# Kernel tuning notes

Measured on AMD Instinct MI355X. Metric: run time of the kernel, lower is better.

## Reference

```python
import jax, jax.numpy as jnp
import numpy as np

N = 50000    # num nodes
E = 800000   # num edges
B = 256      # num graphs
AD, BD = 39, 10          # atom / bond feature dims
H, HEADS, HD, L, TD = 128, 4, 32, 3, 128  # hidden, heads, head_dim, layers, time_dim
BN_EPS = 1e-5


def setup_inputs() -> dict:
    key = jax.random.key(0)
    ks = jax.random.split(key, 24)
    g = lambda i, shape: jax.random.normal(ks[i], shape, dtype=jnp.float32) * 0.05
    return {
        "x": jax.random.normal(ks[0], (N, AD), dtype=jnp.float32),
        "edge_index": jax.random.randint(ks[1], (2, E), 0, N),
        "edge_attr": jax.random.normal(ks[2], (E, BD), dtype=jnp.float32),
        "batch": jnp.sort(jax.random.randint(ks[3], (N,), 0, B)),
        "t": jax.random.randint(ks[4], (B,), 0, 1000),
        "atom_W": g(5, (AD, H)), "atom_b": jnp.zeros((H,), jnp.float32),
        "bond_W": g(6, (BD, H)), "bond_b": jnp.zeros((H,), jnp.float32),
        "lin_W": g(7, (L, H, H)), "edge_W": g(8, (L, H, H)),
        "att_src": g(9, (L, HEADS, HD)), "att_dst": g(10, (L, HEADS, HD)),
        "att_edge": g(11, (L, HEADS, HD)), "conv_b": jnp.zeros((L, H), jnp.float32),
        "bn_gamma": jnp.ones((L, H), jnp.float32), "bn_beta": jnp.zeros((L, H), jnp.float32),
        "out_W": g(12, (H, H)), "out_b": jnp.zeros((H,), jnp.float32),
        "time_W1": g(13, (TD, H)), "time_b1": jnp.zeros((H,), jnp.float32),
        "time_W2": g(14, (H, H)), "time_b2": jnp.zeros((H,), jnp.float32),
        "pool_W1": g(15, (H, H)), "pool_b1": jnp.zeros((H,), jnp.float32),
        "pool_W2": g(16, (H, H)), "pool_b2": jnp.zeros((H,), jnp.float32),
        "np_W1": g(17, (2 * H, H)), "np_b1": jnp.zeros((H,), jnp.float32),
        "np_W2": g(18, (H, H)), "np_b2": jnp.zeros((H,), jnp.float32),
        "np_W3": g(19, (H, AD)), "np_b3": jnp.zeros((AD,), jnp.float32),
    }


def _time_embedding(tf):
    half = TD // 2
    freqs = jnp.exp(jnp.arange(half, dtype=jnp.float32) * (-np.log(10000.0) / (half - 1)))
    e = tf[:, None] * freqs[None, :]
    return jnp.concatenate([jnp.sin(e), jnp.cos(e)], axis=-1)


def _gat_layer(h, e_emb, src, dst, W, We, a_src, a_dst, a_edge, bias):
    # PyG GATConv: shared lin for src/dst, edge features modulate attention only.
    xh = (h @ W).reshape(N, HEADS, HD)
    eh = (e_emb @ We).reshape(E, HEADS, HD)
    s_src = jnp.sum(xh * a_src, axis=-1)    # [N, HEADS]
    s_dst = jnp.sum(xh * a_dst, axis=-1)    # [N, HEADS]
    s_edge = jnp.sum(eh * a_edge, axis=-1)  # [E, HEADS]
    alpha = jax.nn.leaky_relu(s_src[src] + s_dst[dst] + s_edge, 0.2)  # [E, HEADS]
    amax = jax.ops.segment_max(alpha, dst, num_segments=N)
    amax = jnp.where(jnp.isfinite(amax), amax, 0.0)
    ea = jnp.exp(alpha - amax[dst])
    denom = jax.ops.segment_sum(ea, dst, num_segments=N)
    w = ea / (denom[dst] + 1e-16)           # segment softmax over incoming edges
    msg = xh[src] * w[:, :, None]           # [E, HEADS, HD]
    return jax.ops.segment_sum(msg, dst, num_segments=N).reshape(N, H) + bias


def reference(x, edge_index, edge_attr, batch, t,
              atom_W, atom_b, bond_W, bond_b,
              lin_W, edge_W, att_src, att_dst, att_edge, conv_b, bn_gamma, bn_beta,
              out_W, out_b, time_W1, time_b1, time_W2, time_b2,
              pool_W1, pool_b1, pool_W2, pool_b2,
              np_W1, np_b1, np_W2, np_b2, np_W3, np_b3):
    src, dst = edge_index[0], edge_index[1]
    # time conditioning
    t_emb = _time_embedding(t.astype(jnp.float32))
    t_emb = jax.nn.silu(t_emb @ time_W1 + time_b1) @ time_W2 + time_b2  # [B, H]
    # GNN backbone
    h = x @ atom_W + atom_b
    e_emb = edge_attr @ bond_W + bond_b
    for i in range(L):
        h_in = h
        h = _gat_layer(h, e_emb, src, dst, lin_W[i], edge_W[i],
                       att_src[i], att_dst[i], att_edge[i], conv_b[i])
        mu = h.mean(axis=0)
        var = h.var(axis=0)
        h = (h - mu) / jnp.sqrt(var + BN_EPS) * bn_gamma[i] + bn_beta[i]
        h = jax.nn.relu(h)
        h = h + h_in  # residual (dropout is eval-mode identity)
    node_features = h @ out_W + out_b  # [N, H]
    # graph mean pool + pooling MLP
    counts = jnp.clip(jax.ops.segment_sum(jnp.ones((N,), h.dtype), batch, num_segments=B), 1.0, None)
    graph = jax.ops.segment_sum(node_features, batch, num_segments=B) / counts[:, None]
    graph = jax.nn.silu(graph @ pool_W1 + pool_b1) @ pool_W2 + pool_b2  # [B, H]
    tg = t_emb + graph
    # per-node noise prediction
    z = jnp.concatenate([node_features, tg[batch]], axis=-1)  # [N, 2H]
    z = jax.nn.silu(z @ np_W1 + np_b1)
    z = jax.nn.silu(z @ np_W2 + np_b2)
    return z @ np_W3 + np_b3  # [N, AD]
```

## Files before the change

kernel.cpp:

```cpp
#include <hip/hip_runtime.h>
#include <hip/hip_fp16.h>
#include <math.h>

#define N_NODES 50000
#define N_EDGES 800000
#define NB 256
#define AD 39
#define BD 10
#define H 128
#define HEADS 4
#define HD 32
#define LAYERS 3
#define TD 128
#define NBUCK 196
#define EPB 4096

typedef _Float16 f16x8 __attribute__((ext_vector_type(8)));
typedef float f32x4 __attribute__((ext_vector_type(4)));

__device__ __forceinline__ float silu_f(float x) { return x / (1.f + __expf(-x)); }

__device__ __forceinline__ void fma_rank1(float acc[8][4], float4 aL, float4 aH, float4 w)
{
    float ar[8] = {aL.x, aL.y, aL.z, aL.w, aH.x, aH.y, aH.z, aH.w};
    float wr[4] = {w.x, w.y, w.z, w.w};
#pragma unroll
    for (int r = 0; r < 8; r++)
#pragma unroll
        for (int j = 0; j < 4; j++) acc[r][j] += ar[r] * wr[j];
}

template<int KT>
__global__ __launch_bounds__(256) void gemm128(
    const float* __restrict__ A, const float* __restrict__ W,
    const float* __restrict__ bias, float* __restrict__ out,
    int Nrows, int ldw)
{
    __shared__ float As[KT * 68];
    const int tid = threadIdx.x;
    const int rowBase = blockIdx.x * 64;

    for (int idx = tid; idx < 64 * KT; idx += 256) {
        int row = idx / KT;
        int k = idx - row * KT;
        int n = rowBase + row;
        As[k * 68 + row] = (n < Nrows) ? A[(size_t)n * KT + k] : 0.f;
    }
    __syncthreads();

    const int c0 = (tid & 31) * 4;
    const int n0 = (tid >> 5) * 8;

    float acc[8][4];
#pragma unroll
    for (int r = 0; r < 8; r++)
#pragma unroll
        for (int j = 0; j < 4; j++) acc[r][j] = 0.f;

    const float* wp = W + c0;
    int k = 0;
    for (; k + 4 <= KT; k += 4) {
        float4 w0 = *(const float4*)&wp[(size_t)(k + 0) * ldw];
        float4 w1 = *(const float4*)&wp[(size_t)(k + 1) * ldw];
        float4 w2 = *(const float4*)&wp[(size_t)(k + 2) * ldw];
        float4 w3 = *(const float4*)&wp[(size_t)(k + 3) * ldw];
        float4 aL0 = *(const float4*)&As[(k + 0) * 68 + n0];
        float4 aH0 = *(const float4*)&As[(k + 0) * 68 + n0 + 4];
        float4 aL1 = *(const float4*)&As[(k + 1) * 68 + n0];
        float4 aH1 = *(const float4*)&As[(k + 1) * 68 + n0 + 4];
        float4 aL2 = *(const float4*)&As[(k + 2) * 68 + n0];
        float4 aH2 = *(const float4*)&As[(k + 2) * 68 + n0 + 4];
        float4 aL3 = *(const float4*)&As[(k + 3) * 68 + n0];
        float4 aH3 = *(const float4*)&As[(k + 3) * 68 + n0 + 4];
        fma_rank1(acc, aL0, aH0, w0);
        fma_rank1(acc, aL1, aH1, w1);
        fma_rank1(acc, aL2, aH2, w2);
        fma_rank1(acc, aL3, aH3, w3);
    }
    for (; k < KT; ++k) {
        float4 w0 = *(const float4*)&wp[(size_t)k * ldw];
        float4 aL = *(const float4*)&As[k * 68 + n0];
        float4 aH = *(const float4*)&As[k * 68 + n0 + 4];
        fma_rank1(acc, aL, aH, w0);
    }

    float4 bv = make_float4(0.f, 0.f, 0.f, 0.f);
    if (bias) bv = *(const float4*)&bias[c0];

#pragma unroll
    for (int r = 0; r < 8; r++) {
        int n = rowBase + n0 + r;
        if (n >= Nrows) break;
        float4 o;
        o.x = acc[r][0] + bv.x;
        o.y = acc[r][1] + bv.y;
        o.z = acc[r][2] + bv.z;
        o.w = acc[r][3] + bv.w;
        *(float4*)&out[(size_t)n * H + c0] = o;
    }
}

__global__ __launch_bounds__(256) void convert_w_frags(
    const float* __restrict__ lin_W, const float* __restrict__ out_W,
    __half* __restrict__ w16)
{
    int tid = blockIdx.x * 256 + threadIdx.x;
    if (tid >= 4 * H * H) return;
    int mat = tid >> 14;
    int rem = tid & 16383;
    int k = rem >> 7;
    int n = rem & 127;
    const float* src = (mat < 3) ? (lin_W + (size_t)mat * H * H) : out_W;
    float v = src[(size_t)k * H + n];
    int ks = k >> 5, kr = k & 31;
    int lane = ((kr >> 3) << 4) | (n & 15);
    int j = kr & 7;
    int nb = n >> 4;
    w16[(size_t)mat * 16384 + (((ks * 8 + nb) * 64 + lane) << 3) + j] = __float2half(v);
}

__global__ __launch_bounds__(256) void convert_np_frags(
    const float* __restrict__ npW1, const float* __restrict__ npW2,
    const float* __restrict__ npW3, __half* __restrict__ wnp)
{
    int tid = blockIdx.x * 256 + threadIdx.x;
    const int TOT12 = 2 * H * H;
    if (tid < TOT12) {
        int mat = tid >> 14;
        int rem = tid & 16383;
        int k = rem >> 7;
        int n = rem & 127;
        const float* src = mat ? npW2 : npW1;
        float v = src[(size_t)k * H + n];
        int ks = k >> 5, kr = k & 31;
        int lane = ((kr >> 3) << 4) | (n & 15);
        int j = kr & 7;
        int nb = n >> 4;
        wnp[(size_t)mat * 16384 + (((ks * 8 + nb) * 64 + lane) << 3) + j] = __float2half(v);
    } else {
        int r = tid - TOT12;
        if (r >= H * 48) return;
        int k = r / 48;
        int n = r - k * 48;
        float v = (n < AD) ? npW3[(size_t)k * AD + n] : 0.f;
        int ks = k >> 5, kr = k & 31;
        int lane = ((kr >> 3) << 4) | (n & 15);
        int j = kr & 7;
        int nb = n >> 4;
        wnp[32768 + (((ks * 3 + nb) * 64 + lane) << 3) + j] = __float2half(v);
    }
}

__global__ __launch_bounds__(256) void gemm_mfma_bn(
    const float* __restrict__ A,
    const __half* __restrict__ agg, const float* __restrict__ scale,
    const float* __restrict__ shift, float* __restrict__ hio,
    const __half* __restrict__ wfrag, const float* __restrict__ bias,
    float* __restrict__ out32, __half* __restrict__ out16,
    const float* __restrict__ attS, const float* __restrict__ attD,
    float* __restrict__ sS, float* __restrict__ sD, int Nrows)
{
    __shared__ __half Ah[64 * 136];
    const int tid = threadIdx.x;
    const int rowBase = blockIdx.x * 64;

    for (int idx = tid; idx < 64 * 32; idx += 256) {
        int row = idx >> 5;
        int kq = (idx & 31) * 4;
        int n = rowBase + row;
        float4 v = make_float4(0.f, 0.f, 0.f, 0.f);
        if (n < Nrows) {
            if (agg) {
                uint2 u = *(const uint2*)&agg[(size_t)n * H + kq];
                float2 lo = __half22float2(*(__half2*)&u.x);
                float2 hi = __half22float2(*(__half2*)&u.y);
                float4 sc = *(const float4*)&scale[kq];
                float4 sh = *(const float4*)&shift[kq];
                float4 hv = *(const float4*)&hio[(size_t)n * H + kq];
                v.x = fmaxf(lo.x * sc.x + sh.x, 0.f) + hv.x;
                v.y = fmaxf(lo.y * sc.y + sh.y, 0.f) + hv.y;
                v.z = fmaxf(hi.x * sc.z + sh.z, 0.f) + hv.z;
                v.w = fmaxf(hi.y * sc.w + sh.w, 0.f) + hv.w;
                *(float4*)&hio[(size_t)n * H + kq] = v;
            } else {
                v = *(const float4*)&A[(size_t)n * H + kq];
            }
        }
        __half2 a = __floats2half2_rn(v.x, v.y);
        __half2 b = __floats2half2_rn(v.z, v.w);
        *(uint2*)&Ah[row * 136 + kq] = make_uint2(*(unsigned*)&a, *(unsigned*)&b);
    }
    __syncthreads();

    const int wave = tid >> 6;
    const int lane = tid & 63;
    const int lrow = lane & 15;
    const int lgrp = lane >> 4;

    f16x8 bf[4][2];
#pragma unroll
    for (int ks = 0; ks < 4; ks++)
#pragma unroll
        for (int nt = 0; nt < 2; nt++) {
            int nb = wave * 2 + nt;
            bf[ks][nt] = *(const f16x8*)&wfrag[(((ks * 8 + nb) * 64 + lane) << 3)];
        }

    f32x4 acc[4][2];
#pragma unroll
    for (int mt = 0; mt < 4; mt++)
#pragma unroll
        for (int nt = 0; nt < 2; nt++) acc[mt][nt] = (f32x4){0.f, 0.f, 0.f, 0.f};

#pragma unroll
    for (int ks = 0; ks < 4; ks++) {
#pragma unroll
        for (int mt = 0; mt < 4; mt++) {
            f16x8 af = *(const f16x8*)&Ah[(mt * 16 + lrow) * 136 + ks * 32 + lgrp * 8];
            acc[mt][0] = __builtin_amdgcn_mfma_f32_16x16x32_f16(af, bf[ks][0], acc[mt][0], 0, 0, 0);
            acc[mt][1] = __builtin_amdgcn_mfma_f32_16x16x32_f16(af, bf[ks][1], acc[mt][1], 0, 0, 0);
        }
    }

    const int col0 = wave * 32 + lrow;
    const int col1 = col0 + 16;
    float b0 = bias ? bias[col0] : 0.f;
    float b1 = bias ? bias[col1] : 0.f;
    float aS0 = 0.f, aS1 = 0.f, aD0 = 0.f, aD1 = 0.f;
    if (sS) {
        aS0 = attS[col0]; aS1 = attS[col1];
        aD0 = attD[col0]; aD1 = attD[col1];
    }

#pragma unroll
    for (int mt = 0; mt < 4; mt++) {
#pragma unroll
        for (int reg = 0; reg < 4; reg++) {
            int row = rowBase + mt * 16 + lgrp * 4 + reg;
            float v0 = acc[mt][0][reg] + b0;
            float v1 = acc[mt][1][reg] + b1;
            if (row < Nrows) {
                if (out16) {
                    out16[(size_t)row * H + col0] = __float2half(v0);
                    out16[(size_t)row * H + col1] = __float2half(v1);
                } else {
                    out32[(size_t)row * H + col0] = v0;
                    out32[(size_t)row * H + col1] = v1;
                }
            }
            if (sS) {
                float ps = v0 * aS0 + v1 * aS1;
                float pd = v0 * aD0 + v1 * aD1;
#pragma unroll
                for (int off = 8; off >= 1; off >>= 1) {
                    ps += __shfl_xor(ps, off, 16);
                    pd += __shfl_xor(pd, off, 16);
                }
                if (lrow == 0 && row < Nrows) {
                    sS[row * 4 + wave] = ps;
                    sD[row * 4 + wave] = pd;
                }
            }
        }
    }
}

__global__ __launch_bounds__(256) void np_fused_mfma(
    const float* __restrict__ nf, const int* __restrict__ batch,
    const float* __restrict__ tgW, const __half* __restrict__ wnp,
    const float* __restrict__ npb2, const float* __restrict__ npb3,
    float* __restrict__ out, int Nrows)
{
    __shared__ __half Ah[64 * 136];
    const int tid = threadIdx.x;
    const int rowBase = blockIdx.x * 64;

    for (int idx = tid; idx < 64 * 32; idx += 256) {
        int row = idx >> 5;
        int kq = (idx & 31) * 4;
        int n = rowBase + row;
        float4 v = make_float4(0.f, 0.f, 0.f, 0.f);
        if (n < Nrows) v = *(const float4*)&nf[(size_t)n * H + kq];
        __half2 a = __floats2half2_rn(v.x, v.y);
        __half2 b = __floats2half2_rn(v.z, v.w);
        *(uint2*)&Ah[row * 136 + kq] = make_uint2(*(unsigned*)&a, *(unsigned*)&b);
    }
    __syncthreads();

    const int wave = tid >> 6;
    const int lane = tid & 63;
    const int lrow = lane & 15;
    const int lgrp = lane >> 4;

    f32x4 acc[4][2];

    {
        f16x8 bf[4][2];
#pragma unroll
        for (int ks = 0; ks < 4; ks++)
#pragma unroll
            for (int nt = 0; nt < 2; nt++) {
                int nb = wave * 2 + nt;
                bf[ks][nt] = *(const f16x8*)&wnp[(((ks * 8 + nb) * 64 + lane) << 3)];
            }
#pragma unroll
        for (int mt = 0; mt < 4; mt++)
#pragma unroll
            for (int nt = 0; nt < 2; nt++) acc[mt][nt] = (f32x4){0.f, 0.f, 0.f, 0.f};
#pragma unroll
        for (int ks = 0; ks < 4; ks++) {
#pragma unroll
            for (int mt = 0; mt < 4; mt++) {
                f16x8 af = *(const f16x8*)&Ah[(mt * 16 + lrow) * 136 + ks * 32 + lgrp * 8];
                acc[mt][0] = __builtin_amdgcn_mfma_f32_16x16x32_f16(af, bf[ks][0], acc[mt][0], 0, 0, 0);
                acc[mt][1] = __builtin_amdgcn_mfma_f32_16x16x32_f16(af, bf[ks][1], acc[mt][1], 0, 0, 0);
            }
        }
    }
    __syncthreads();

#pragma unroll
    for (int mt = 0; mt < 4; mt++) {
#pragma unroll
        for (int nt = 0; nt < 2; nt++) {
            int col = wave * 32 + nt * 16 + lrow;
#pragma unroll
            for (int reg = 0; reg < 4; reg++) {
                int row = mt * 16 + lgrp * 4 + reg;
                int n = rowBase + row;
                float v = acc[mt][nt][reg];
                if (n < Nrows) v += tgW[(size_t)batch[n] * H + col];
                Ah[row * 136 + col] = __float2half(silu_f(v));
            }
        }
    }
    __syncthreads();

    {
        const __half* w2 = wnp + 16384;
        f16x8 bf[4][2];
#pragma unroll
        for (int ks = 0; ks < 4; ks++)
#pragma unroll
            for (int nt = 0; nt < 2; nt++) {
                int nb = wave * 2 + nt;
                bf[ks][nt] = *(const f16x8*)&w2[(((ks * 8 + nb) * 64 + lane) << 3)];
            }
#pragma unroll
        for (int mt = 0; mt < 4; mt++)
#pragma unroll
            for (int nt = 0; nt < 2; nt++) acc[mt][nt] = (f32x4){0.f, 0.f, 0.f, 0.f};
#pragma unroll
        for (int ks = 0; ks < 4; ks++) {
#pragma unroll
            for (int mt = 0; mt < 4; mt++) {
                f16x8 af = *(const f16x8*)&Ah[(mt * 16 + lrow) * 136 + ks * 32 + lgrp * 8];
                acc[mt][0] = __builtin_amdgcn_mfma_f32_16x16x32_f16(af, bf[ks][0], acc[mt][0], 0, 0, 0);
                acc[mt][1] = __builtin_amdgcn_mfma_f32_16x16x32_f16(af, bf[ks][1], acc[mt][1], 0, 0, 0);
            }
        }
    }
    __syncthreads();

#pragma unroll
    for (int mt = 0; mt < 4; mt++) {
#pragma unroll
        for (int nt = 0; nt < 2; nt++) {
            int col = wave * 32 + nt * 16 + lrow;
            float b2 = npb2[col];
#pragma unroll
            for (int reg = 0; reg < 4; reg++) {
                int row = mt * 16 + lgrp * 4 + reg;
                Ah[row * 136 + col] = __float2half(silu_f(acc[mt][nt][reg] + b2));
            }
        }
    }
    __syncthreads();

    {
        const __half* w3 = wnp + 32768;
        f32x4 acc3[3];
#pragma unroll
        for (int nt = 0; nt < 3; nt++) acc3[nt] = (f32x4){0.f, 0.f, 0.f, 0.f};
#pragma unroll
        for (int ks = 0; ks < 4; ks++) {
            f16x8 af = *(const f16x8*)&Ah[(wave * 16 + lrow) * 136 + ks * 32 + lgrp * 8];
#pragma unroll
            for (int nt = 0; nt < 3; nt++) {
                f16x8 bf = *(const f16x8*)&w3[(((ks * 3 + nt) * 64 + lane) << 3)];
                acc3[nt] = __builtin_amdgcn_mfma_f32_16x16x32_f16(af, bf, acc3[nt], 0, 0, 0);
            }
        }
#pragma unroll
        for (int nt = 0; nt < 3; nt++) {
            int col = nt * 16 + lrow;
            if (col < AD) {
                float b3 = npb3[col];
#pragma unroll
                for (int reg = 0; reg < 4; reg++) {
                    int row = rowBase + wave * 16 + lgrp * 4 + reg;
                    if (row < Nrows) out[(size_t)row * AD + col] = acc3[nt][reg] + b3;
                }
            }
        }
    }
}

__global__ __launch_bounds__(256) void precompute_small(
    const float* __restrict__ edge_W, const float* __restrict__ att_edge,
    const float* __restrict__ bond_W, const float* __restrict__ bond_b,
    float* __restrict__ mc)
{
    __shared__ float bl[LAYERS][H][4];
    int tid = threadIdx.x;
    for (int task = tid; task < LAYERS * H; task += 256) {
        int l = task / H, k = task % H;
#pragma unroll
        for (int hh = 0; hh < 4; hh++) {
            float s = 0.f;
            for (int d = 0; d < HD; d++)
                s += edge_W[(size_t)l * H * H + k * H + hh * HD + d] *
                     att_edge[l * H + hh * HD + d];
            bl[l][k][hh] = s;
        }
    }
    __syncthreads();
    if (tid < LAYERS * BD * 4) {
        int l = tid / (BD * 4), r = tid % (BD * 4), j = r / 4, hh = r % 4;
        float s = 0.f;
        for (int k = 0; k < H; k++) s += bond_W[j * H + k] * bl[l][k][hh];
        mc[l * 44 + j * 4 + hh] = s;
    }
    if (tid >= 128 && tid < 128 + LAYERS * 4) {
        int r = tid - 128, l = r / 4, hh = r % 4;
        float s = 0.f;
        for (int k = 0; k < H; k++) s += bond_b[k] * bl[l][k][hh];
        mc[l * 44 + 40 + hh] = s;
    }
}

__global__ __launch_bounds__(128) void time_embed(
    const int* __restrict__ t,
    const float* __restrict__ W1, const float* __restrict__ b1,
    const float* __restrict__ W2, const float* __restrict__ b2,
    float* __restrict__ t_emb)
{
    int g = blockIdx.x, c = threadIdx.x;
    float tf = (float)t[g];
    __shared__ float emb[TD], z[H];
    int k = c & 63;
    float f = __expf(-9.210340371976184f * (float)k / 63.0f);
    float e = tf * f;
    emb[c] = (c < 64) ? sinf(e) : cosf(e);
    __syncthreads();
    float a1 = b1[c];
    for (int kk = 0; kk < TD; kk++) a1 += emb[kk] * W1[kk * H + c];
    z[c] = silu_f(a1);
    __syncthreads();
    float a2 = b2[c];
    for (int kk = 0; kk < H; kk++) a2 += z[kk] * W2[kk * H + c];
    t_emb[g * H + c] = a2;
}

__global__ __launch_bounds__(256) void hist_dst(const int* __restrict__ edge_index,
                                                int* __restrict__ deg)
{
    int e = blockIdx.x * 256 + threadIdx.x;
    if (e < N_EDGES) atomicAdd(&deg[edge_index[N_EDGES + e]], 1);
}

__global__ __launch_bounds__(320) void gptr_bsearch(const int* __restrict__ batch,
                                                    int* __restrict__ gptr)
{
    int g = threadIdx.x;
    if (g > NB) return;
    int lo = 0, hi = N_NODES;
    while (lo < hi) {
        int mid = (lo + hi) >> 1;
        if (batch[mid] < g) lo = mid + 1; else hi = mid;
    }
    gptr[g] = lo;
}

__global__ __launch_bounds__(256) void scan_part(const int* __restrict__ cnt,
                                                 int* __restrict__ bsum, int n)
{
    int tid = threadIdx.x;
    int i0 = blockIdx.x * 1024 + tid * 4;
    int s = 0;
#pragma unroll
    for (int j = 0; j < 4; j++) if (i0 + j < n) s += cnt[i0 + j];
    __shared__ int red[256];
    red[tid] = s;
    __syncthreads();
    for (int off = 128; off >= 1; off >>= 1) {
        if (tid < off) red[tid] += red[tid + off];
        __syncthreads();
    }
    if (tid == 0) bsum[blockIdx.x] = red[0];
}

__global__ __launch_bounds__(256) void scan_tops(const int* __restrict__ bsum,
                                                 int* __restrict__ boff, int G,
                                                 int* __restrict__ total)
{
    int tid = threadIdx.x;
    int v = (tid < G) ? bsum[tid] : 0;
    __shared__ int ps[256];
    ps[tid] = v;
    __syncthreads();
    for (int off = 1; off < 256; off <<= 1) {
        int t = (tid >= off) ? ps[tid - off] : 0;
        __syncthreads();
        ps[tid] += t;
        __syncthreads();
    }
    if (tid < G) boff[tid] = ps[tid] - v;
    if (tid == 255) *total = ps[255];
}

__global__ __launch_bounds__(256) void scan_final(const int* __restrict__ cnt,
                                                  const int* __restrict__ boff,
                                                  int* __restrict__ ptr, int n)
{
    int tid = threadIdx.x;
    int i0 = blockIdx.x * 1024 + tid * 4;
    int v[4];
#pragma unroll
    for (int j = 0; j < 4; j++) v[j] = (i0 + j < n) ? cnt[i0 + j] : 0;
    int s = v[0] + v[1] + v[2] + v[3];
    __shared__ int ps[256];
    ps[tid] = s;
    __syncthreads();
    for (int off = 1; off < 256; off <<= 1) {
        int t = (tid >= off) ? ps[tid - off] : 0;
        __syncthreads();
        ps[tid] += t;
        __syncthreads();
    }
    int run = boff[blockIdx.x] + ps[tid] - s;
#pragma unroll
    for (int j = 0; j < 4; j++) {
        if (i0 + j < n) { ptr[i0 + j] = run; run += v[j]; }
    }
}

__global__ __launch_bounds__(256) void init_gcur(const int* __restrict__ csr_ptr,
                                                 int* __restrict__ gcur)
{
    int b = threadIdx.x;
    if (b < NBUCK) gcur[b] = csr_ptr[min(b << 8, N_NODES)];
}

__global__ __launch_bounds__(256) void bucket_scatter_a(
    const int* __restrict__ edge_index, int* __restrict__ gcur,
    int4* __restrict__ tmp)
{
    __shared__ int cnt[NBUCK], cbase[NBUCK], cur[NBUCK];
    const int tid = threadIdx.x;
    const int e0 = blockIdx.x * EPB;
    for (int i = tid; i < NBUCK; i += 256) { cnt[i] = 0; cur[i] = 0; }
    __syncthreads();
    for (int i = 0; i < EPB; i += 256) {
        int e = e0 + i + tid;
        if (e < N_EDGES) atomicAdd(&cnt[edge_index[N_EDGES + e] >> 8], 1);
    }
    __syncthreads();
    for (int i = tid; i < NBUCK; i += 256)
        if (cnt[i] > 0) cbase[i] = atomicAdd(&gcur[i], cnt[i]);
    __syncthreads();
    for (int i = 0; i < EPB; i += 256) {
        int e = e0 + i + tid;
        if (e < N_EDGES) {
            int s = edge_index[e];
            int d = edge_index[N_EDGES + e];
            int b = d >> 8;
            int off = atomicAdd(&cur[b], 1);
            tmp[cbase[b] + off] = make_int4(s, e, d, 0);
        }
    }
}

__global__ __launch_bounds__(256) void bucket_scatter_b(
    const int4* __restrict__ tmp, const int* __restrict__ csr_ptr,
    int2* __restrict__ csr_se)
{
    __shared__ int lcur[256];
    const int b = blockIdx.x;
    const int n0 = b << 8;
    const int tid = threadIdx.x;
    lcur[tid] = 0;
    __syncthreads();
    int start = csr_ptr[n0];
    int end   = csr_ptr[min(n0 + 256, N_NODES)];
    for (int p = start + tid; p < end; p += 256) {
        int4 q = tmp[p];
        int pos = atomicAdd(&lcur[q.z - n0], 1);
        csr_se[csr_ptr[q.z] + pos] = make_int2(q.x, q.y);
    }
}

__global__ __launch_bounds__(256) void ase_csr(
    const int2* __restrict__ csr_se, const float* __restrict__ edge_attr,
    const float* __restrict__ sS, const float* __restrict__ mc_l,
    __half* __restrict__ ase)
{
    __shared__ float Ml[BD * 4], cl[4];
    int tid = threadIdx.x;
    if (tid < 40) Ml[tid] = mc_l[tid];
    if (tid >= 40 && tid < 44) cl[tid - 40] = mc_l[tid];
    __syncthreads();
    int p = blockIdx.x * 256 + tid;
    if (p >= N_EDGES) return;
    int2 q = csr_se[p];
    float4 ss = *(const float4*)&sS[q.x * 4];
    float s0 = cl[0] + ss.x, s1 = cl[1] + ss.y;
    float s2 = cl[2] + ss.z, s3 = cl[3] + ss.w;
    const float* ea = &edge_attr[(size_t)q.y * BD];
#pragma unroll
    for (int j = 0; j < BD; j++) {
        float x = ea[j];
        s0 += x * Ml[j * 4 + 0]; s1 += x * Ml[j * 4 + 1];
        s2 += x * Ml[j * 4 + 2]; s3 += x * Ml[j * 4 + 3];
    }
    __half2 h01 = __floats2half2_rn(s0, s1);
    __half2 h23 = __floats2half2_rn(s2, s3);
    uint2 u = make_uint2(*(const unsigned*)&h01, *(const unsigned*)&h23);
    *(uint2*)&ase[(size_t)p * 4] = u;
}

__global__ __launch_bounds__(256) void gat_agg_full(
    const __half* __restrict__ xh16, const __half* __restrict__ ase,
    const int* __restrict__ csr_ptr, const int2* __restrict__ csr_se,
    const float* __restrict__ sD, const float* __restrict__ conv_b_l,
    __half* __restrict__ agg)
{
    int n = (blockIdx.x * 256 + threadIdx.x) >> 6;
    if (n >= N_NODES) return;
    int lane = threadIdx.x & 63;
    int c0 = lane * 2;
    int hd = lane >> 4;
    int start = csr_ptr[n], end = csr_ptr[n + 1];
    float sDn = sD[n * 4 + hd];

    float m_run = -1e30f, d_run = 0.f;
    float acc0 = 0.f, acc1 = 0.f;

    for (int base = start; base < end; base += 64) {
        int cnt = min(64, end - base);
        int s_l = (lane < cnt) ? csr_se[base + lane].x : 0;

        float a_t[4], e_t[4];
        float m_blk = -1e30f;
#pragma unroll
        for (int t = 0; t < 4; t++) {
            int i = (lane & 15) + t * 16;
            float a = -1e30f;
            if (i < cnt) {
                a = __half2float(ase[(size_t)(base + i) * 4 + hd]) + sDn;
                a = (a >= 0.f) ? a : 0.2f * a;
            }
            a_t[t] = a;
            m_blk = fmaxf(m_blk, a);
        }
#pragma unroll
        for (int off = 8; off >= 1; off >>= 1)
            m_blk = fmaxf(m_blk, __shfl_xor(m_blk, off, 16));
        float m_new = fmaxf(m_run, m_blk);
        float rescale = __expf(m_run - m_new);
        float dsum = 0.f;
#pragma unroll
        for (int t = 0; t < 4; t++) {
            e_t[t] = __expf(a_t[t] - m_new);
            dsum += e_t[t];
        }
#pragma unroll
        for (int off = 8; off >= 1; off >>= 1)
            dsum += __shfl_xor(dsum, off, 16);
        d_run = d_run * rescale + dsum;
        acc0 *= rescale;
        acc1 *= rescale;

        int srcb = lane & 48;
#pragma unroll
        for (int t = 0; t < 4; t++) {
            int rem = cnt - t * 16;
            if (rem <= 0) break;
            int lim = min(16, (rem + 3) & ~3);
            for (int i2 = 0; i2 < lim; i2 += 4) {
                int i = t * 16 + i2;
                int s0 = __shfl(s_l, i + 0), s1 = __shfl(s_l, i + 1);
                int s2 = __shfl(s_l, i + 2), s3 = __shfl(s_l, i + 3);
                float w0 = __shfl(e_t[t], srcb | (i2 + 0));
                float w1 = __shfl(e_t[t], srcb | (i2 + 1));
                float w2 = __shfl(e_t[t], srcb | (i2 + 2));
                float w3 = __shfl(e_t[t], srcb | (i2 + 3));
                float2 x0 = __half22float2(*(const __half2*)&xh16[(size_t)s0 * H + c0]);
                float2 x1 = __half22float2(*(const __half2*)&xh16[(size_t)s1 * H + c0]);
                float2 x2 = __half22float2(*(const __half2*)&xh16[(size_t)s2 * H + c0]);
                float2 x3 = __half22float2(*(const __half2*)&xh16[(size_t)s3 * H + c0]);
                acc0 += x0.x * w0 + x1.x * w1 + x2.x * w2 + x3.x * w3;
                acc1 += x0.y * w0 + x1.y * w1 + x2.y * w2 + x3.y * w3;
            }
        }
        m_run = m_new;
    }
    float inv = 1.f / (d_run + 1e-16f);
    __half2 o = __floats2half2_rn(acc0 * inv + conv_b_l[c0],
                                  acc1 * inv + conv_b_l[c0 + 1]);
    *(__half2*)&agg[(size_t)n * H + c0] = o;
}

__global__ __launch_bounds__(256) void bn_partial_f(const __half* __restrict__ agg,
                                                    float* __restrict__ part)
{
    const int PER = (N_NODES + 511) / 512;
    __shared__ float red[2][8][128];
    int b = blockIdx.x;
    int cg = threadIdx.x & 31;
    int rs = threadIdx.x >> 5;
    int c4 = cg * 4;
    int s = b * PER, e = min(N_NODES, s + PER);
    float s0 = 0.f, s1 = 0.f, s2 = 0.f, s3 = 0.f;
    float q0 = 0.f, q1 = 0.f, q2 = 0.f, q3 = 0.f;
    for (int n = s + rs; n < e; n += 8) {
        uint2 u = *(const uint2*)&agg[(size_t)n * H + c4];
        float2 lo = __half22float2(*(__half2*)&u.x);
        float2 hi = __half22float2(*(__half2*)&u.y);
        s0 += lo.x; q0 += lo.x * lo.x;
        s1 += lo.y; q1 += lo.y * lo.y;
        s2 += hi.x; q2 += hi.x * hi.x;
        s3 += hi.y; q3 += hi.y * hi.y;
    }
    *(float4*)&red[0][rs][c4] = make_float4(s0, s1, s2, s3);
    *(float4*)&red[1][rs][c4] = make_float4(q0, q1, q2, q3);
    __syncthreads();
    if (threadIdx.x < 128) {
        int c = threadIdx.x;
        float sum = 0.f, sq = 0.f;
#pragma unroll
        for (int r = 0; r < 8; r++) { sum += red[0][r][c]; sq += red[1][r][c]; }
        part[b * H + c] = sum;
        part[512 * H + b * H + c] = sq;
    }
}

__global__ __launch_bounds__(256) void bn_finish_f(const float* __restrict__ part,
                                                   const float* __restrict__ gamma,
                                                   const float* __restrict__ beta,
                                                   float* __restrict__ scale,
                                                   float* __restrict__ shift)
{
    __shared__ double red[2][2][128];
    int c = threadIdx.x & 127;
    int g = threadIdx.x >> 7;
    double s = 0.0, q = 0.0;
    for (int b = g * 256; b < (g + 1) * 256; b++) {
        s += (double)part[b * H + c];
        q += (double)part[512 * H + b * H + c];
    }
    red[0][g][c] = s;
    red[1][g][c] = q;
    __syncthreads();
    if (g == 0) {
        s = red[0][0][c] + red[0][1][c];
        q = red[1][0][c] + red[1][1][c];
        float mu = (float)(s / N_NODES);
        float var = (float)(q / N_NODES) - mu * mu;
        float rstd = rsqrtf(var + 1e-5f);
        float sc = gamma[c] * rstd;
        scale[c] = sc;
        shift[c] = beta[c] - mu * sc;
    }
}

__global__ __launch_bounds__(128) void pool_partial(
    const float* __restrict__ nf, const int* __restrict__ gptr,
    float* __restrict__ pprt)
{
    int g = blockIdx.x >> 2;
    int q = blockIdx.x & 3;
    int c = threadIdx.x;
    int s = gptr[g], e = gptr[g + 1];
    int qlen = (e - s + 3) >> 2;
    int qs = s + q * qlen;
    int qe = min(e, qs + qlen);
    float sum = 0.f;
    for (int n = qs; n < qe; n++) sum += nf[(size_t)n * H + c];
    pprt[((size_t)g * 4 + q) * H + c] = sum;
}

__global__ __launch_bounds__(512) void graph_head_mlp(
    const int* __restrict__ gptr, const float* __restrict__ pprt,
    const float* __restrict__ t_emb,
    const float* __restrict__ pW1, const float* __restrict__ pb1,
    const float* __restrict__ pW2, const float* __restrict__ pb2,
    const float* __restrict__ npW1, const float* __restrict__ npb1,
    float* __restrict__ tgW)
{
    int g = blockIdx.x;
    int c = threadIdx.x & 127;
    int q = threadIdx.x >> 7;
    __shared__ float row[H], z[H];
    __shared__ float red[4][H];

    int s = gptr[g], e = gptr[g + 1];
    float cf = (e - s > 0) ? (float)(e - s) : 1.f;
    if (q == 0) {
        row[c] = (pprt[((size_t)g * 4 + 0) * H + c] +
                  pprt[((size_t)g * 4 + 1) * H + c] +
                  pprt[((size_t)g * 4 + 2) * H + c] +
                  pprt[((size_t)g * 4 + 3) * H + c]) / cf;
    }
    __syncthreads();

    float p = 0.f;
#pragma unroll 8
    for (int k = q * 32; k < q * 32 + 32; k++) p += row[k] * pW1[k * H + c];
    red[q][c] = p;
    __syncthreads();
    if (q == 0) z[c] = silu_f(red[0][c] + red[1][c] + red[2][c] + red[3][c] + pb1[c]);
    __syncthreads();

    p = 0.f;
#pragma unroll 8
    for (int k = q * 32; k < q * 32 + 32; k++) p += z[k] * pW2[k * H + c];
    red[q][c] = p;
    __syncthreads();
    if (q == 0) row[c] = red[0][c] + red[1][c] + red[2][c] + red[3][c] + pb2[c]
                         + t_emb[g * H + c];
    __syncthreads();

    p = 0.f;
#pragma unroll 8
    for (int k = q * 32; k < q * 32 + 32; k++)
        p += row[k] * npW1[(size_t)(128 + k) * H + c];
    red[q][c] = p;
    __syncthreads();
    if (q == 0) tgW[g * H + c] = red[0][c] + red[1][c] + red[2][c] + red[3][c] + npb1[c];
}

extern "C" void kernel_launch(void* const* d_in, const int* in_sizes, int n_in,
                              void* d_out, int out_size, void* d_ws, size_t ws_size,
                              hipStream_t stream)
{
    const float* x          = (const float*)d_in[0];
    const int*   edge_index = (const int*)d_in[1];
    const float* edge_attr  = (const float*)d_in[2];
    const int*   batch      = (const int*)d_in[3];
    const int*   t          = (const int*)d_in[4];
    const float* atom_W     = (const float*)d_in[5];
    const float* atom_b     = (const float*)d_in[6];
    const float* bond_W     = (const float*)d_in[7];
    const float* bond_b     = (const float*)d_in[8];
    const float* lin_W      = (const float*)d_in[9];
    const float* edge_W     = (const float*)d_in[10];
    const float* att_src    = (const float*)d_in[11];
    const float* att_dst    = (const float*)d_in[12];
    const float* att_edge   = (const float*)d_in[13];
    const float* conv_b     = (const float*)d_in[14];
    const float* bn_gamma   = (const float*)d_in[15];
    const float* bn_beta    = (const float*)d_in[16];
    const float* out_W      = (const float*)d_in[17];
    const float* out_b      = (const float*)d_in[18];
    const float* time_W1    = (const float*)d_in[19];
    const float* time_b1    = (const float*)d_in[20];
    const float* time_W2    = (const float*)d_in[21];
    const float* time_b2    = (const float*)d_in[22];
    const float* pool_W1    = (const float*)d_in[23];
    const float* pool_b1    = (const float*)d_in[24];
    const float* pool_W2    = (const float*)d_in[25];
    const float* pool_b2    = (const float*)d_in[26];
    const float* np_W1      = (const float*)d_in[27];
    const float* np_b1      = (const float*)d_in[28];
    const float* np_W2      = (const float*)d_in[29];
    const float* np_b2      = (const float*)d_in[30];
    const float* np_W3      = (const float*)d_in[31];
    const float* np_b3      = (const float*)d_in[32];

    const size_t OFF_H     = 0;
    const size_t OFF_XH    = 6400000;
    const size_t OFF_AGG   = 12800000;
    const size_t OFF_ASE   = 16000000;
    const size_t OFF_SD    = 17600000;
    const size_t OFF_TEMB  = 17800000;
    const size_t OFF_TGW   = 17832768;
    const size_t OFF_MC    = 17865536;
    const size_t OFF_BNSC  = 17865792;
    const size_t OFF_BNSH  = 17865920;
    const size_t OFF_PART  = 17866048;
    const size_t REQ_FLOATS = 17898816;
    const size_t REQ_BYTES  = REQ_FLOATS * 4;

    if (ws_size < REQ_BYTES) {
        hipMemsetAsync(d_out, 0, (size_t)out_size * sizeof(float), stream);
        return;
    }

    float* fws    = (float*)d_ws;
    float* h      = fws + OFF_H;
    float* xh     = fws + OFF_XH;
    __half* xh16  = (__half*)(fws + OFF_XH);
    int4*  etmp   = (int4*)(fws + OFF_XH);
    __half* agg   = (__half*)(fws + OFF_AGG);
    __half* ase   = (__half*)(fws + OFF_ASE);
    float* sD     = fws + OFF_SD;
    float* t_emb  = fws + OFF_TEMB;
    float* tgW    = fws + OFF_TGW;
    float* mc     = fws + OFF_MC;
    float* bnsc   = fws + OFF_BNSC;
    float* bnsh   = fws + OFF_BNSH;
    float* part   = fws + OFF_PART;
    float* pprt   = fws + OFF_AGG;
    __half* wnp   = (__half*)part;

    int* ib       = (int*)d_out;
    int* csr_ptr  = ib;
    int2* csr_se  = (int2*)(ib + 50016);
    int* deg      = ib + 1650016;
    int* gcur     = deg;
    int* gptr     = ib + 1700032;
    int* bsum     = ib + 1700292;
    int* boff     = ib + 1700356;
    float* sS     = (float*)d_out + 1700420;
    float* bnpart = sS;
    __half* w16   = (__half*)((float*)d_out + 1900420);

    hipMemsetAsync(deg, 0, N_NODES * sizeof(int), stream);

    precompute_small<<<1, 256, 0, stream>>>(edge_W, att_edge, bond_W, bond_b, mc);
    time_embed<<<NB, 128, 0, stream>>>(t, time_W1, time_b1, time_W2, time_b2, t_emb);
    gptr_bsearch<<<1, 320, 0, stream>>>(batch, gptr);
    convert_w_frags<<<(4 * H * H + 255) / 256, 256, 0, stream>>>(lin_W, out_W, w16);

    hist_dst<<<(N_EDGES + 255) / 256, 256, 0, stream>>>(edge_index, deg);

    const int GSN = (N_NODES + 1023) / 1024;
    scan_part<<<GSN, 256, 0, stream>>>(deg, bsum, N_NODES);
    scan_tops<<<1, 256, 0, stream>>>(bsum, boff, GSN, &csr_ptr[N_NODES]);
    scan_final<<<GSN, 256, 0, stream>>>(deg, boff, csr_ptr, N_NODES);

    init_gcur<<<1, 256, 0, stream>>>(csr_ptr, gcur);
    bucket_scatter_a<<<(N_EDGES + EPB - 1) / EPB, 256, 0, stream>>>(
        edge_index, gcur, etmp);
    bucket_scatter_b<<<NBUCK, 256, 0, stream>>>(etmp, csr_ptr, csr_se);

    const int GB = (N_NODES + 63) / 64;
    const int GE = (N_EDGES + 255) / 256;

    gemm128<AD><<<GB, 256, 0, stream>>>(x, atom_W, atom_b, h, N_NODES, H);

    for (int l = 0; l < LAYERS; l++) {
        gemm_mfma_bn<<<GB, 256, 0, stream>>>(
            (l == 0) ? h : nullptr,
            (l == 0) ? nullptr : agg, bnsc, bnsh, h,
            w16 + (size_t)l * 16384, nullptr,
            nullptr, xh16,
            att_src + l * H, att_dst + l * H, sS, sD, N_NODES);
        ase_csr<<<GE, 256, 0, stream>>>(csr_se, edge_attr, sS, mc + l * 44, ase);
        gat_agg_full<<<N_NODES / 4, 256, 0, stream>>>(
            xh16, ase, csr_ptr, csr_se, sD, conv_b + l * H, agg);
        bn_partial_f<<<512, 256, 0, stream>>>(agg, bnpart);
        bn_finish_f<<<1, 256, 0, stream>>>(bnpart, bn_gamma + l * H,
                                           bn_beta + l * H, bnsc, bnsh);
    }

    convert_np_frags<<<(2 * H * H + H * 48 + 255) / 256, 256, 0, stream>>>(
        np_W1, np_W2, np_W3, wnp);

    gemm_mfma_bn<<<GB, 256, 0, stream>>>(
        nullptr, agg, bnsc, bnsh, h,
        w16 + (size_t)3 * 16384, out_b,
        xh, nullptr,
        nullptr, nullptr, nullptr, nullptr, N_NODES);

    pool_partial<<<NB * 4, 128, 0, stream>>>(xh, gptr, pprt);
    graph_head_mlp<<<NB, 512, 0, stream>>>(gptr, pprt, t_emb, pool_W1, pool_b1,
                                           pool_W2, pool_b2, np_W1, np_b1, tgW);

    np_fused_mfma<<<GB, 256, 0, stream>>>(xh, batch, tgW, wnp, np_b2, np_b3,
                                          (float*)d_out, N_NODES);
}
```

Baseline: 471.6 us.

## Precompute per-layer edge attention terms once and gather source scores in aggregation

Replaces the per-layer ase_csr kernel with a single pre-pass that computes the edge-attribute attention term for all three layers at once, reading edge_attr once in CSR order. The aggregation kernel now adds the source-node score by gathering sS through a shuffled source index, which removes two launches and the repeated edge_attr gathers. In exchange it needs a larger workspace buffer and adds a random sS gather inside the aggregation inner loop.

```diff
diff --git a/kernel.cpp b/kernel.cpp
--- a/kernel.cpp
+++ b/kernel.cpp
@@ -600,37 +600,41 @@
     }
 }
 
-__global__ __launch_bounds__(256) void ase_csr(
+__global__ __launch_bounds__(256) void se3_pre(
     const int2* __restrict__ csr_se, const float* __restrict__ edge_attr,
-    const float* __restrict__ sS, const float* __restrict__ mc_l,
-    __half* __restrict__ ase)
-{
-    __shared__ float Ml[BD * 4], cl[4];
+    const float* __restrict__ mc, __half* __restrict__ se3)
+{
+    __shared__ float Ml[LAYERS * 44];
     int tid = threadIdx.x;
-    if (tid < 40) Ml[tid] = mc_l[tid];
-    if (tid >= 40 && tid < 44) cl[tid - 40] = mc_l[tid];
+    if (tid < LAYERS * 44) Ml[tid] = mc[tid];
     __syncthreads();
     int p = blockIdx.x * 256 + tid;
     if (p >= N_EDGES) return;
-    int2 q = csr_se[p];
-    float4 ss = *(const float4*)&sS[q.x * 4];
-    float s0 = cl[0] + ss.x, s1 = cl[1] + ss.y;
-    float s2 = cl[2] + ss.z, s3 = cl[3] + ss.w;
-    const float* ea = &edge_attr[(size_t)q.y * BD];
-#pragma unroll
-    for (int j = 0; j < BD; j++) {
-        float x = ea[j];
-        s0 += x * Ml[j * 4 + 0]; s1 += x * Ml[j * 4 + 1];
-        s2 += x * Ml[j * 4 + 2]; s3 += x * Ml[j * 4 + 3];
-    }
-    __half2 h01 = __floats2half2_rn(s0, s1);
-    __half2 h23 = __floats2half2_rn(s2, s3);
-    uint2 u = make_uint2(*(const unsigned*)&h01, *(const unsigned*)&h23);
-    *(uint2*)&ase[(size_t)p * 4] = u;
+    int e = csr_se[p].y;
+    float ea[BD];
+    const float* eap = &edge_attr[(size_t)e * BD];
+#pragma unroll
+    for (int j = 0; j < BD; j++) ea[j] = eap[j];
+#pragma unroll
+    for (int l = 0; l < LAYERS; l++) {
+        const float* M = &Ml[l * 44];
+        float s0 = M[40], s1 = M[41], s2 = M[42], s3 = M[43];
+#pragma unroll
+        for (int j = 0; j < BD; j++) {
+            float x = ea[j];
+            s0 += x * M[j * 4 + 0]; s1 += x * M[j * 4 + 1];
+            s2 += x * M[j * 4 + 2]; s3 += x * M[j * 4 + 3];
+        }
+        __half2 h01 = __floats2half2_rn(s0, s1);
+        __half2 h23 = __floats2half2_rn(s2, s3);
+        uint2 u = make_uint2(*(const unsigned*)&h01, *(const unsigned*)&h23);
+        *(uint2*)&se3[((size_t)l * N_EDGES + p) * 4] = u;
+    }
 }
 
 __global__ __launch_bounds__(256) void gat_agg_full(
-    const __half* __restrict__ xh16, const __half* __restrict__ ase,
+    const __half* __restrict__ xh16, const __half* __restrict__ se3l,
+    const float* __restrict__ sS,
     const int* __restrict__ csr_ptr, const int2* __restrict__ csr_se,
     const float* __restrict__ sD, const float* __restrict__ conv_b_l,
     __half* __restrict__ agg)
@@ -657,7 +661,9 @@
             int i = (lane & 15) + t * 16;
             float a = -1e30f;
             if (i < cnt) {
-                a = __half2float(ase[(size_t)(base + i) * 4 + hd]) + sDn;
+                int src = __shfl(s_l, i);
+                a = sS[src * 4 + hd] +
+                    __half2float(se3l[(size_t)(base + i) * 4 + hd]) + sDn;
                 a = (a >= 0.f) ? a : 0.2f * a;
             }
             a_t[t] = a;
@@ -889,7 +895,8 @@
     const size_t OFF_BNSC  = 17865792;
     const size_t OFF_BNSH  = 17865920;
     const size_t OFF_PART  = 17866048;
-    const size_t REQ_FLOATS = 17898816;
+    const size_t OFF_SE3   = 17898816;
+    const size_t REQ_FLOATS = 22698816;
     const size_t REQ_BYTES  = REQ_FLOATS * 4;
 
     if (ws_size < REQ_BYTES) {
@@ -903,7 +910,6 @@
     __half* xh16  = (__half*)(fws + OFF_XH);
     int4*  etmp   = (int4*)(fws + OFF_XH);
     __half* agg   = (__half*)(fws + OFF_AGG);
-    __half* ase   = (__half*)(fws + OFF_ASE);
     float* sD     = fws + OFF_SD;
     float* t_emb  = fws + OFF_TEMB;
     float* tgW    = fws + OFF_TGW;
@@ -913,6 +919,7 @@
     float* part   = fws + OFF_PART;
     float* pprt   = fws + OFF_AGG;
     __half* wnp   = (__half*)part;
+    __half* se3   = (__half*)(fws + OFF_SE3);
 
     int* ib       = (int*)d_out;
     int* csr_ptr  = ib;
@@ -948,6 +955,8 @@
     const int GB = (N_NODES + 63) / 64;
     const int GE = (N_EDGES + 255) / 256;
 
+    se3_pre<<<GE, 256, 0, stream>>>(csr_se, edge_attr, mc, se3);
+
     gemm128<AD><<<GB, 256, 0, stream>>>(x, atom_W, atom_b, h, N_NODES, H);
 
     for (int l = 0; l < LAYERS; l++) {
@@ -957,9 +966,9 @@
             w16 + (size_t)l * 16384, nullptr,
             nullptr, xh16,
             att_src + l * H, att_dst + l * H, sS, sD, N_NODES);
-        ase_csr<<<GE, 256, 0, stream>>>(csr_se, edge_attr, sS, mc + l * 44, ase);
         gat_agg_full<<<N_NODES / 4, 256, 0, stream>>>(
-            xh16, ase, csr_ptr, csr_se, sD, conv_b + l * H, agg);
+            xh16, se3 + (size_t)l * N_EDGES * 4, sS,
+            csr_ptr, csr_se, sD, conv_b + l * H, agg);
         bn_partial_f<<<512, 256, 0, stream>>>(agg, bnpart);
         bn_finish_f<<<1, 256, 0, stream>>>(bnpart, bn_gamma + l * H,
                                            bn_beta + l * H, bnsc, bnsh);
```

Result: faster. 441.9 us (-6.3%).
